# Optimization experiments

Measured on AMD Instinct MI355X. Metric: run time of the kernel, lower is better.

The kernel has to match this reference:

```python
import jax, jax.numpy as jnp
import numpy as np

# ---- module hyperparameters (from init_kwargs) ----
DIM = 16        # Hilbert-space dimension (density matrix is DIM x DIM)
BATCH = 32      # number of initial states evolved in parallel
K_LIND = 4      # number of Lindblad collapse operators
N_TS = 512      # number of Euler integration steps
N_CTRLS = 4     # number of control channels
N_PARAMS = 16   # B-spline control points per channel
DEGREE = 3      # cubic B-splines
T_TOTAL = 1.0
DT = T_TOTAL / N_TS


def _bspline_basis_matrix(t, knots, degree):
    """Cox-de Boor recursion, vectorized over all basis functions.
    t: (n_ts,), knots: (n_knots,). Returns (n_ts, n_knots-1-degree)."""
    k = knots
    # degree-0: indicator of half-open knot spans -> (n_ts, n_knots-1)
    B = ((k[None, :-1] <= t[:, None]) & (t[:, None] < k[None, 1:])).astype(t.dtype)
    for d in range(1, degree + 1):
        left_den = k[d:-1] - k[:-(d + 1)]
        right_den = k[d + 1:] - k[1:-d]
        left = jnp.where(left_den > 0,
                         (t[:, None] - k[None, :-(d + 1)]) / jnp.where(left_den > 0, left_den, 1.0) * B[:, :-1],
                         0.0)
        right = jnp.where(right_den > 0,
                          (k[None, d + 1:] - t[:, None]) / jnp.where(right_den > 0, right_den, 1.0) * B[:, 1:],
                          0.0)
        B = left + right
    return B  # (n_ts, n_knots - 1 - degree) == (n_ts, N_PARAMS)


def setup_inputs() -> dict:
    key = jax.random.key(0)
    ks = jax.random.split(key, 10)
    f32 = jnp.float32
    params = 0.5 * jax.random.normal(ks[0], (N_PARAMS, N_CTRLS), f32)
    H0_re = jax.random.normal(ks[1], (DIM, DIM), f32)
    H0_im = jax.random.normal(ks[2], (DIM, DIM), f32)
    Hc_re = jax.random.normal(ks[3], (N_CTRLS, DIM, DIM), f32)
    Hc_im = jax.random.normal(ks[4], (N_CTRLS, DIM, DIM), f32)
    L_re = 0.3 * jax.random.normal(ks[5], (K_LIND, DIM, DIM), f32)
    L_im = 0.3 * jax.random.normal(ks[6], (K_LIND, DIM, DIM), f32)
    # valid density matrices: rho0 = A A^dag / tr(A A^dag)
    A = (jax.random.normal(ks[7], (BATCH, DIM, DIM), f32)
         + 1j * jax.random.normal(ks[8], (BATCH, DIM, DIM), f32)).astype(jnp.complex64)
    rho0 = jnp.einsum('bij,bkj->bik', A, A.conj())
    tr = jnp.trace(rho0, axis1=-2, axis2=-1).real[:, None, None]
    rho0 = rho0 / tr.astype(jnp.complex64)
    return {
        'params': params,
        'H0_re': H0_re, 'H0_im': H0_im,
        'Hc_re': Hc_re, 'Hc_im': Hc_im,
        'L_re': L_re, 'L_im': L_im,
        'rho0_re': jnp.real(rho0).astype(f32),
        'rho0_im': jnp.imag(rho0).astype(f32),
    }


def reference(params, H0_re, H0_im, Hc_re, Hc_im, L_re, L_im, rho0_re, rho0_im):
    c64 = jnp.complex64
    # Hermitize Hamiltonians
    H0 = (H0_re + 1j * H0_im).astype(c64)
    H0 = 0.5 * (H0 + H0.conj().T)
    Hc = (Hc_re + 1j * Hc_im).astype(c64)
    Hc = 0.5 * (Hc + jnp.conj(jnp.swapaxes(Hc, -1, -2)))
    L = (L_re + 1j * L_im).astype(c64)              # (K, d, d)
    LdL = jnp.einsum('kji,kjl->il', L.conj(), L)    # sum_k L^dag L  (d, d)
    rho0 = (rho0_re + 1j * rho0_im).astype(c64)     # (B, d, d)

    # B-spline control pulses (clamped knot vector, as in evaluate_bspline_batch)
    t = jnp.arange(N_TS, dtype=jnp.float32) * DT
    knots = jnp.concatenate([
        jnp.zeros(DEGREE, jnp.float32),
        jnp.linspace(0.0, T_TOTAL, N_PARAMS - DEGREE + 1).astype(jnp.float32),
        T_TOTAL * jnp.ones(DEGREE, jnp.float32),
    ])
    basis = _bspline_basis_matrix(t, knots, DEGREE)  # (n_ts, n_params)
    u = basis @ params                               # (n_ts, n_ctrls)

    def step(rho, u_t):
        H = H0 + jnp.einsum('c,cij->ij', u_t.astype(c64), Hc)
        jump = jnp.einsum('kij,bjl,kml->bim', L, rho, L.conj())
        drho = (-1j) * (H @ rho - rho @ H) + jump - 0.5 * (LdL @ rho + rho @ LdL)
        rho_new = rho + DT * drho
        pops = jnp.real(jnp.diagonal(rho_new, axis1=-2, axis2=-1)).astype(jnp.float32)
        return rho_new, pops

    _, pops = jax.lax.scan(step, rho0, u)
    return pops  # (n_ts, batch, dim) real populations
```

## Files before the change

### kernel.cpp

```cpp
#include <hip/hip_runtime.h>
#include <hip/hip_bf16.h>

#define DIM    16
#define BATCH  32
#define KL     4
#define NTS    512
#define NC     4
#define NPAR   16
#define DTF    (1.0f/512.0f)
#define BST    40
#define FST    20

using short8  = __attribute__((ext_vector_type(8))) short;
using short4v = __attribute__((ext_vector_type(4))) short;
using f32x4   = __attribute__((ext_vector_type(4))) float;

__device__ __forceinline__ float b2f(__hip_bfloat16 x) { return __bfloat162float(x); }

__device__ __forceinline__ float ldval(const void* p, int idx, bool isf32) {
  return isf32 ? ((const float*)p)[idx]
               : __bfloat162float(((const __hip_bfloat16*)p)[idx]);
}
__device__ __forceinline__ unsigned short f2bf(float x) {
  unsigned u = __float_as_uint(x);
  unsigned r = u + 0x7FFFu + ((u >> 16) & 1u);
  return (unsigned short)(r >> 16);
}
__device__ __forceinline__ float bf2f(unsigned short h) {
  return __uint_as_float(((unsigned)h) << 16);
}
__device__ __forceinline__ void split2(float v, unsigned short& h, unsigned short& l) {
  unsigned u = __float_as_uint(v);
  h = (unsigned short)(u >> 16);
  float r = v - __uint_as_float(u & 0xFFFF0000u);
  l = (unsigned short)(__float_as_uint(r) >> 16);
}
__device__ __forceinline__ short8 ldfrag(const unsigned short* p) {
  return *(const short8*)p;
}
__device__ __forceinline__ short8 negbf8(short8 a) {
  union { short8 s; unsigned u[4]; } v; v.s = a;
  #pragma unroll
  for (int q = 0; q < 4; ++q) v.u[q] ^= 0x80008000u;
  return v.s;
}
__device__ __forceinline__ f32x4 mm3(short8 Ah, short8 Al, short8 Bh, short8 Bl, f32x4 acc) {
  acc = __builtin_amdgcn_mfma_f32_16x16x32_bf16(Ah, Bh, acc, 0, 0, 0);
  acc = __builtin_amdgcn_mfma_f32_16x16x32_bf16(Al, Bh, acc, 0, 0, 0);
  acc = __builtin_amdgcn_mfma_f32_16x16x32_bf16(Ah, Bl, acc, 0, 0, 0);
  return acc;
}
__device__ __forceinline__ void packfrag(const float* v, short8& hi, short8& lo) {
  union { short8 s; unsigned short e[8]; } H, L;
  #pragma unroll
  for (int q = 0; q < 8; ++q) split2(v[q], H.e[q], L.e[q]);
  hi = H.s; lo = L.s;
}

__global__ __launch_bounds__(512, 1)
void lindblad_evolve(const void* __restrict__ g_params,
                     const void* __restrict__ g_H0re, const void* __restrict__ g_H0im,
                     const void* __restrict__ g_Hcre, const void* __restrict__ g_Hcim,
                     const void* __restrict__ g_Lre,  const void* __restrict__ g_Lim,
                     const void* __restrict__ g_r0re, const void* __restrict__ g_r0im,
                     float* __restrict__ g_out)
{
  __shared__ __align__(16) unsigned short sPh[16*BST], sPl[16*BST];
  __shared__ __align__(16) unsigned short sTh[KL][16*BST], sTl[KL][16*BST];
  __shared__ __align__(16) unsigned short sLh[KL][16*BST], sLl[KL][16*BST];
  __shared__ __align__(16) float sMr[16*FST],  sMi[16*FST];
  __shared__ __align__(16) float sMrT[16*FST], sMiT[16*FST];
  __shared__ __align__(16) float sU[NTS][NC];
  __shared__ __align__(16) float sPops[NTS*DIM];
  __shared__ int sFlag;

  const int tid = threadIdx.x;
  const int b   = blockIdx.x;
  const int i   = tid >> 4;
  const int j   = tid & 15;
  const int wv  = tid >> 6;
  const int ln  = tid & 63;
  const int fm  = ln & 15;
  const int fq  = ln >> 4;
  const int row0 = fq * 4;
  const int fOff  = fm*BST + fq*8;
  const int fOffS = fm*BST + ((fq*8 + 16) & 31);

  if (tid == 0) sFlag = 0;
  __syncthreads();
  if (tid < 256) {
    float v = b2f(((const __hip_bfloat16*)g_H0re)[tid]);
    if (!(fabsf(v) <= 1e10f)) atomicOr(&sFlag, 1);
  }
  __syncthreads();
  const bool isf32 = (sFlag != 0);

  {
    float kn[20];
    kn[0] = 0.f; kn[1] = 0.f; kn[2] = 0.f;
    #pragma unroll
    for (int q = 0; q < 14; ++q) kn[3 + q] = (float)q / 13.0f;
    kn[17] = 1.f; kn[18] = 1.f; kn[19] = 1.f;
    const int ts = tid;
    const float t = (float)ts * DTF;
    float B[19];
    #pragma unroll
    for (int q = 0; q < 19; ++q) B[q] = (kn[q] <= t && t < kn[q+1]) ? 1.f : 0.f;
    #pragma unroll
    for (int d = 1; d <= 3; ++d) {
      #pragma unroll
      for (int q = 0; q + d < 19; ++q) {
        float ld = kn[q+d]   - kn[q];
        float rd = kn[q+d+1] - kn[q+1];
        float lv = (ld > 0.f) ? (t - kn[q])     / ld * B[q]   : 0.f;
        float rv = (rd > 0.f) ? (kn[q+d+1] - t) / rd * B[q+1] : 0.f;
        B[q] = lv + rv;
      }
    }
    #pragma unroll
    for (int c = 0; c < NC; ++c) {
      float s = 0.f;
      #pragma unroll
      for (int q = 0; q < NPAR; ++q) s += B[q] * ldval(g_params, q*NC + c, isf32);
      sU[ts][c] = s;
    }
  }

  if (tid < 256) {
    float* scr = sPops;
    const int ij = i*16 + j, ji = j*16 + i;
    float h0r = 0.5f * (ldval(g_H0re, ij, isf32) + ldval(g_H0re, ji, isf32));
    float h0i = 0.5f * (ldval(g_H0im, ij, isf32) - ldval(g_H0im, ji, isf32));
    float ldr = 0.f, ldi = 0.f;
    for (int k = 0; k < KL; ++k) {
      #pragma unroll
      for (int m = 0; m < DIM; ++m) {
        float ar = ldval(g_Lre, k*256 + m*16 + i, isf32), ai = ldval(g_Lim, k*256 + m*16 + i, isf32);
        float br = ldval(g_Lre, k*256 + m*16 + j, isf32), bi = ldval(g_Lim, k*256 + m*16 + j, isf32);
        ldr += ar*br + ai*bi;
        ldi += ar*bi - ai*br;
      }
    }
    scr[0*256 + ij] =  h0i - 0.5f*ldr;
    scr[1*256 + ij] = -h0r - 0.5f*ldi;
    #pragma unroll
    for (int c = 0; c < NC; ++c) {
      float hr = 0.5f * (ldval(g_Hcre, c*256 + ij, isf32) + ldval(g_Hcre, c*256 + ji, isf32));
      float hi = 0.5f * (ldval(g_Hcim, c*256 + ij, isf32) - ldval(g_Hcim, c*256 + ji, isf32));
      scr[(2 + 2*c)*256 + ij] =  hi;
      scr[(3 + 2*c)*256 + ij] = -hr;
    }
    #pragma unroll
    for (int k = 0; k < KL; ++k) {
      float lr = ldval(g_Lre, k*256 + ij, isf32);
      float li = ldval(g_Lim, k*256 + ij, isf32);
      unsigned short h;
      h = f2bf(lr); sLh[k][i*BST + j]      = h; sLl[k][i*BST + j]      = f2bf(lr - bf2f(h));
      h = f2bf(li); sLh[k][i*BST + 16 + j] = h; sLl[k][i*BST + 16 + j] = f2bf(li - bf2f(h));
    }
    float r0 = ldval(g_r0re, b*256 + ij, isf32);
    float m0 = ldval(g_r0im, b*256 + ij, isf32);
    unsigned short h, l;
    split2(r0, h, l); sPh[j*BST + i]      = h; sPl[j*BST + i]      = l;
    split2(m0, h, l); sPh[j*BST + 16 + i] = h; sPl[j*BST + 16 + i] = l;
  }

  __syncthreads();

  short8 Ah, Al;
  short8 JBh[KL], JBl[KL];
  float  G0v[8], Gcv[NC][8];
  float  rm[4] = {0.f,0.f,0.f,0.f};

  if (wv < 2) {
    const int comp = (fq < 2) ? 0 : 1;
    const int base = (fq & 1) * 8;
    const float* scr = sPops;
    {
      const float* s0 = &scr[comp*256 + fm*16 + base];
      f32x4 va = *(const f32x4*)s0, vb = *(const f32x4*)(s0 + 4);
      G0v[0]=va[0]; G0v[1]=va[1]; G0v[2]=va[2]; G0v[3]=va[3];
      G0v[4]=vb[0]; G0v[5]=vb[1]; G0v[6]=vb[2]; G0v[7]=vb[3];
    }
    #pragma unroll
    for (int c = 0; c < NC; ++c) {
      const float* s0 = &scr[(2 + 2*c + comp)*256 + fm*16 + base];
      f32x4 va = *(const f32x4*)s0, vb = *(const f32x4*)(s0 + 4);
      Gcv[c][0]=va[0]; Gcv[c][1]=va[1]; Gcv[c][2]=va[2]; Gcv[c][3]=va[3];
      Gcv[c][4]=vb[0]; Gcv[c][5]=vb[1]; Gcv[c][6]=vb[2]; Gcv[c][7]=vb[3];
    }
    f32x4 uv = *(const f32x4*)&sU[0][0];
    float gv[8];
    #pragma unroll
    for (int q = 0; q < 8; ++q)
      gv[q] = G0v[q] + uv[0]*Gcv[0][q] + uv[1]*Gcv[1][q] + uv[2]*Gcv[2][q] + uv[3]*Gcv[3][q];
    packfrag(gv, Ah, Al);
  } else if (wv < 6) {
    const int k = wv - 2;
    Ah = ldfrag(&sLh[k][fOff]);
    Al = ldfrag(&sLl[k][fOff]);
  } else if (wv == 6) {
    #pragma unroll
    for (int k = 0; k < KL; ++k) { JBh[k] = ldfrag(&sLh[k][fOff]); JBl[k] = ldfrag(&sLl[k][fOff]); }
    #pragma unroll
    for (int q = 0; q < 4; ++q) rm[q] = ldval(g_r0re, b*256 + (row0+q)*16 + fm, isf32);
  } else {
    #pragma unroll
    for (int k = 0; k < KL; ++k) {
      short8 h = ldfrag(&sLh[k][fOffS]);
      short8 l = ldfrag(&sLl[k][fOffS]);
      if (fq < 2) { h = negbf8(h); l = negbf8(l); }
      JBh[k] = h; JBl[k] = l;
    }
    #pragma unroll
    for (int q = 0; q < 4; ++q) rm[q] = ldval(g_r0im, b*256 + (row0+q)*16 + fm, isf32);
  }

  #pragma unroll 1
  for (int t = 0; t < NTS; ++t) {
    __syncthreads();

    if (wv < 2) {
      short8 Bh, Bl;
      if (wv == 0) {
        Bh = ldfrag(&sPh[fOff]);  Bl = ldfrag(&sPl[fOff]);
        if (fq >= 2) { Bh = negbf8(Bh); Bl = negbf8(Bl); }
      } else {
        Bh = ldfrag(&sPh[fOffS]); Bl = ldfrag(&sPl[fOffS]);
      }
      f32x4 a = {0.f,0.f,0.f,0.f};
      a = mm3(Ah, Al, Bh, Bl, a);
      float* Mn = (wv == 0) ? sMr  : sMi;
      float* Mt = (wv == 0) ? sMrT : sMiT;
      #pragma unroll
      for (int r = 0; r < 4; ++r) Mn[(row0 + r)*FST + fm] = a[r];
      *(f32x4*)&Mt[fm*FST + row0] = a;
      const int tn = (t + 1 < NTS) ? (t + 1) : t;
      f32x4 uv = *(const f32x4*)&sU[tn][0];
      float gv[8];
      #pragma unroll
      for (int q = 0; q < 8; ++q)
        gv[q] = G0v[q] + uv[0]*Gcv[0][q] + uv[1]*Gcv[1][q] + uv[2]*Gcv[2][q] + uv[3]*Gcv[3][q];
      packfrag(gv, Ah, Al);
    } else if (wv < 6) {
      const int k = wv - 2;
      short8 Brh = ldfrag(&sPh[fOff]),  Brl = ldfrag(&sPl[fOff]);
      if (fq >= 2) { Brh = negbf8(Brh); Brl = negbf8(Brl); }
      short8 Bih = ldfrag(&sPh[fOffS]), Bil = ldfrag(&sPl[fOffS]);
      f32x4 ar = {0.f,0.f,0.f,0.f}, ai = {0.f,0.f,0.f,0.f};
      ar = mm3(Ah, Al, Brh, Brl, ar);
      ai = mm3(Ah, Al, Bih, Bil, ai);
      #pragma unroll
      for (int r = 0; r < 4; ++r) {
        unsigned short h, l;
        split2(ar[r], h, l);
        sTh[k][(row0 + r)*BST + fm]      = h;
        sTl[k][(row0 + r)*BST + fm]      = l;
        split2(ai[r], h, l);
        sTh[k][(row0 + r)*BST + 16 + fm] = h;
        sTl[k][(row0 + r)*BST + 16 + fm] = l;
      }
    }

    __syncthreads();

    if (wv >= 6) {
      f32x4 a0 = {0.f,0.f,0.f,0.f}, a1 = {0.f,0.f,0.f,0.f},
            a2 = {0.f,0.f,0.f,0.f}, a3 = {0.f,0.f,0.f,0.f};
      a0 = mm3(ldfrag(&sTh[0][fOff]), ldfrag(&sTl[0][fOff]), JBh[0], JBl[0], a0);
      a1 = mm3(ldfrag(&sTh[1][fOff]), ldfrag(&sTl[1][fOff]), JBh[1], JBl[1], a1);
      a2 = mm3(ldfrag(&sTh[2][fOff]), ldfrag(&sTl[2][fOff]), JBh[2], JBl[2], a2);
      a3 = mm3(ldfrag(&sTh[3][fOff]), ldfrag(&sTl[3][fOff]), JBh[3], JBl[3], a3);
      const float* Mt = (wv == 6) ? sMrT : sMiT;
      const float* Mn = (wv == 6) ? sMr  : sMi;
      f32x4 d1 = *(const f32x4*)&Mt[fm*FST + row0];
      f32x4 d2 = *(const f32x4*)&Mn[fm*FST + row0];
      union { short4v s; unsigned short e[4]; } HH, LL;
      if (wv == 6) {
        #pragma unroll
        for (int q = 0; q < 4; ++q) {
          rm[q] += DTF * (d1[q] + d2[q] + ((a0[q] + a1[q]) + (a2[q] + a3[q])));
          split2(rm[q], HH.e[q], LL.e[q]);
        }
        *(short4v*)&sPh[fm*BST + row0] = HH.s;
        *(short4v*)&sPl[fm*BST + row0] = LL.s;
        if ((unsigned)(fm - row0) < 4u) sPops[t*DIM + fm] = rm[fm - row0];
      } else {
        #pragma unroll
        for (int q = 0; q < 4; ++q) {
          rm[q] += DTF * (d1[q] - d2[q] + ((a0[q] + a1[q]) + (a2[q] + a3[q])));
          split2(rm[q], HH.e[q], LL.e[q]);
        }
        *(short4v*)&sPh[fm*BST + 16 + row0] = HH.s;
        *(short4v*)&sPl[fm*BST + 16 + row0] = LL.s;
      }
    }
  }

  __syncthreads();
  #pragma unroll
  for (int s = 0; s < NTS*DIM/512; ++s) {
    int idx = s*512 + tid;
    g_out[(idx >> 4)*(BATCH*DIM) + b*DIM + (idx & 15)] = sPops[idx];
  }
}

extern "C" void kernel_launch(void* const* d_in, const int* in_sizes, int n_in,
                              void* d_out, int out_size, void* d_ws, size_t ws_size,
                              hipStream_t stream) {
  (void)out_size; (void)d_ws; (void)ws_size;
  const void *P, *H0r, *H0i, *Hcr, *Hci, *Lr, *Li, *R0r, *R0i;
  int idx64 = -1;
  for (int q = 0; q < n_in; ++q) if (in_sizes[q] == 64) idx64 = q;
  if (idx64 == 6) {
    H0i = d_in[0]; H0r = d_in[1];
    Hci = d_in[2]; Hcr = d_in[3];
    Li  = d_in[4]; Lr  = d_in[5];
    P   = d_in[6];
    R0i = d_in[7]; R0r = d_in[8];
  } else {
    P   = d_in[0];
    H0r = d_in[1]; H0i = d_in[2];
    Hcr = d_in[3]; Hci = d_in[4];
    Lr  = d_in[5]; Li  = d_in[6];
    R0r = d_in[7]; R0i = d_in[8];
  }
  lindblad_evolve<<<dim3(BATCH), dim3(512), 0, stream>>>(
      P, H0r, H0i, Hcr, Hci, Lr, Li, R0r, R0i, (float*)d_out);
}
```

Before: 422.1 us.

## Fold final update into Hamiltonian waves and rebalance jump products across waves

After: 441.1 us. 1.04x slower.

```diff
diff --git a/kernel.cpp b/kernel.cpp
--- a/kernel.cpp
+++ b/kernel.cpp
@@ -10,6 +10,7 @@
 #define DTF    (1.0f/512.0f)
 #define BST    40
 #define FST    20
+#define TST    36
 
 using short8  = __attribute__((ext_vector_type(8))) short;
 using short4v = __attribute__((ext_vector_type(4))) short;
@@ -35,6 +36,11 @@
   float r = v - __uint_as_float(u & 0xFFFF0000u);
   l = (unsigned short)(__float_as_uint(r) >> 16);
 }
+__device__ __forceinline__ unsigned splitpack(float v) {
+  unsigned short h, l;
+  split2(v, h, l);
+  return (unsigned)h | ((unsigned)l << 16);
+}
 __device__ __forceinline__ short8 ldfrag(const unsigned short* p) {
   return *(const short8*)p;
 }
@@ -54,6 +60,20 @@
   union { short8 s; unsigned short e[8]; } H, L;
   #pragma unroll
   for (int q = 0; q < 8; ++q) split2(v[q], H.e[q], L.e[q]);
+  hi = H.s; lo = L.s;
+}
+__device__ __forceinline__ void ldfrag_paired(const unsigned* p, short8& hi, short8& lo) {
+  uint4 wa = *(const uint4*)p;
+  uint4 wb = *(const uint4*)(p + 4);
+  union { short8 s; unsigned u[4]; } H, L;
+  H.u[0] = __builtin_amdgcn_perm(wa.y, wa.x, 0x05040100u);
+  H.u[1] = __builtin_amdgcn_perm(wa.w, wa.z, 0x05040100u);
+  H.u[2] = __builtin_amdgcn_perm(wb.y, wb.x, 0x05040100u);
+  H.u[3] = __builtin_amdgcn_perm(wb.w, wb.z, 0x05040100u);
+  L.u[0] = __builtin_amdgcn_perm(wa.y, wa.x, 0x07060302u);
+  L.u[1] = __builtin_amdgcn_perm(wa.w, wa.z, 0x07060302u);
+  L.u[2] = __builtin_amdgcn_perm(wb.y, wb.x, 0x07060302u);
+  L.u[3] = __builtin_amdgcn_perm(wb.w, wb.z, 0x07060302u);
   hi = H.s; lo = L.s;
 }
 
@@ -66,10 +86,9 @@
                      float* __restrict__ g_out)
 {
   __shared__ __align__(16) unsigned short sPh[16*BST], sPl[16*BST];
-  __shared__ __align__(16) unsigned short sTh[KL][16*BST], sTl[KL][16*BST];
+  __shared__ __align__(16) unsigned sTp[KL][16*TST];
   __shared__ __align__(16) unsigned short sLh[KL][16*BST], sLl[KL][16*BST];
-  __shared__ __align__(16) float sMr[16*FST],  sMi[16*FST];
-  __shared__ __align__(16) float sMrT[16*FST], sMiT[16*FST];
+  __shared__ __align__(16) float sMr[16*FST], sMi[16*FST];
   __shared__ __align__(16) float sU[NTS][NC];
   __shared__ __align__(16) float sPops[NTS*DIM];
   __shared__ int sFlag;
@@ -101,8 +120,7 @@
     #pragma unroll
     for (int q = 0; q < 14; ++q) kn[3 + q] = (float)q / 13.0f;
     kn[17] = 1.f; kn[18] = 1.f; kn[19] = 1.f;
-    const int ts = tid;
-    const float t = (float)ts * DTF;
+    const float t = (float)tid * DTF;
     float B[19];
     #pragma unroll
     for (int q = 0; q < 19; ++q) B[q] = (kn[q] <= t && t < kn[q+1]) ? 1.f : 0.f;
@@ -122,7 +140,7 @@
       float s = 0.f;
       #pragma unroll
       for (int q = 0; q < NPAR; ++q) s += B[q] * ldval(g_params, q*NC + c, isf32);
-      sU[ts][c] = s;
+      sU[tid][c] = s;
     }
   }
 
@@ -179,15 +197,15 @@
     {
       const float* s0 = &scr[comp*256 + fm*16 + base];
       f32x4 va = *(const f32x4*)s0, vb = *(const f32x4*)(s0 + 4);
-      G0v[0]=va[0]; G0v[1]=va[1]; G0v[2]=va[2]; G0v[3]=va[3];
-      G0v[4]=vb[0]; G0v[5]=vb[1]; G0v[6]=vb[2]; G0v[7]=vb[3];
+      #pragma unroll
+      for (int q = 0; q < 4; ++q) { G0v[q] = va[q]; G0v[4+q] = vb[q]; }
     }
     #pragma unroll
     for (int c = 0; c < NC; ++c) {
       const float* s0 = &scr[(2 + 2*c + comp)*256 + fm*16 + base];
       f32x4 va = *(const f32x4*)s0, vb = *(const f32x4*)(s0 + 4);
-      Gcv[c][0]=va[0]; Gcv[c][1]=va[1]; Gcv[c][2]=va[2]; Gcv[c][3]=va[3];
-      Gcv[c][4]=vb[0]; Gcv[c][5]=vb[1]; Gcv[c][6]=vb[2]; Gcv[c][7]=vb[3];
+      #pragma unroll
+      for (int q = 0; q < 4; ++q) { Gcv[c][q] = va[q]; Gcv[c][4+q] = vb[q]; }
     }
     f32x4 uv = *(const f32x4*)&sU[0][0];
     float gv[8];
@@ -195,31 +213,33 @@
     for (int q = 0; q < 8; ++q)
       gv[q] = G0v[q] + uv[0]*Gcv[0][q] + uv[1]*Gcv[1][q] + uv[2]*Gcv[2][q] + uv[3]*Gcv[3][q];
     packfrag(gv, Ah, Al);
-  } else if (wv < 6) {
-    const int k = wv - 2;
+    if (wv == 0) {
+      #pragma unroll
+      for (int k = 0; k < KL; ++k) { JBh[k] = ldfrag(&sLh[k][fOff]); JBl[k] = ldfrag(&sLl[k][fOff]); }
+      #pragma unroll
+      for (int q = 0; q < 4; ++q) rm[q] = ldval(g_r0re, b*256 + (row0+q)*16 + fm, isf32);
+    } else {
+      #pragma unroll
+      for (int k = 0; k < KL; ++k) {
+        short8 h = ldfrag(&sLh[k][fOffS]);
+        short8 l = ldfrag(&sLl[k][fOffS]);
+        if (fq < 2) { h = negbf8(h); l = negbf8(l); }
+        JBh[k] = h; JBl[k] = l;
+      }
+      #pragma unroll
+      for (int q = 0; q < 4; ++q) rm[q] = ldval(g_r0im, b*256 + (row0+q)*16 + fm, isf32);
+    }
+  } else {
+    const int k = (wv < 6) ? (wv - 2) : (wv - 4);
     Ah = ldfrag(&sLh[k][fOff]);
     Al = ldfrag(&sLl[k][fOff]);
-  } else if (wv == 6) {
-    #pragma unroll
-    for (int k = 0; k < KL; ++k) { JBh[k] = ldfrag(&sLh[k][fOff]); JBl[k] = ldfrag(&sLl[k][fOff]); }
-    #pragma unroll
-    for (int q = 0; q < 4; ++q) rm[q] = ldval(g_r0re, b*256 + (row0+q)*16 + fm, isf32);
-  } else {
-    #pragma unroll
-    for (int k = 0; k < KL; ++k) {
-      short8 h = ldfrag(&sLh[k][fOffS]);
-      short8 l = ldfrag(&sLl[k][fOffS]);
-      if (fq < 2) { h = negbf8(h); l = negbf8(l); }
-      JBh[k] = h; JBl[k] = l;
-    }
-    #pragma unroll
-    for (int q = 0; q < 4; ++q) rm[q] = ldval(g_r0im, b*256 + (row0+q)*16 + fm, isf32);
   }
 
   #pragma unroll 1
   for (int t = 0; t < NTS; ++t) {
     __syncthreads();
 
+    f32x4 d1 = {0.f,0.f,0.f,0.f};
     if (wv < 2) {
       short8 Bh, Bl;
       if (wv == 0) {
@@ -228,13 +248,10 @@
       } else {
         Bh = ldfrag(&sPh[fOffS]); Bl = ldfrag(&sPl[fOffS]);
       }
-      f32x4 a = {0.f,0.f,0.f,0.f};
-      a = mm3(Ah, Al, Bh, Bl, a);
-      float* Mn = (wv == 0) ? sMr  : sMi;
-      float* Mt = (wv == 0) ? sMrT : sMiT;
-      #pragma unroll
-      for (int r = 0; r < 4; ++r) Mn[(row0 + r)*FST + fm] = a[r];
-      *(f32x4*)&Mt[fm*FST + row0] = a;
+      d1 = mm3(Ah, Al, Bh, Bl, d1);
+      float* Mn = (wv == 0) ? sMr : sMi;
+      #pragma unroll
+      for (int r = 0; r < 4; ++r) Mn[(row0 + r)*FST + fm] = d1[r];
       const int tn = (t + 1 < NTS) ? (t + 1) : t;
       f32x4 uv = *(const f32x4*)&sU[tn][0];
       float gv[8];
@@ -242,41 +259,54 @@
       for (int q = 0; q < 8; ++q)
         gv[q] = G0v[q] + uv[0]*Gcv[0][q] + uv[1]*Gcv[1][q] + uv[2]*Gcv[2][q] + uv[3]*Gcv[3][q];
       packfrag(gv, Ah, Al);
-    } else if (wv < 6) {
-      const int k = wv - 2;
-      short8 Brh = ldfrag(&sPh[fOff]),  Brl = ldfrag(&sPl[fOff]);
-      if (fq >= 2) { Brh = negbf8(Brh); Brl = negbf8(Brl); }
-      short8 Bih = ldfrag(&sPh[fOffS]), Bil = ldfrag(&sPl[fOffS]);
-      f32x4 ar = {0.f,0.f,0.f,0.f}, ai = {0.f,0.f,0.f,0.f};
-      ar = mm3(Ah, Al, Brh, Brl, ar);
-      ai = mm3(Ah, Al, Bih, Bil, ai);
-      #pragma unroll
-      for (int r = 0; r < 4; ++r) {
-        unsigned short h, l;
-        split2(ar[r], h, l);
-        sTh[k][(row0 + r)*BST + fm]      = h;
-        sTl[k][(row0 + r)*BST + fm]      = l;
-        split2(ai[r], h, l);
-        sTh[k][(row0 + r)*BST + 16 + fm] = h;
-        sTl[k][(row0 + r)*BST + 16 + fm] = l;
+    } else {
+      const int k = (wv < 6) ? (wv - 2) : (wv - 4);
+      if (wv < 4) {
+        short8 Brh = ldfrag(&sPh[fOff]),  Brl = ldfrag(&sPl[fOff]);
+        if (fq >= 2) { Brh = negbf8(Brh); Brl = negbf8(Brl); }
+        short8 Bih = ldfrag(&sPh[fOffS]), Bil = ldfrag(&sPl[fOffS]);
+        f32x4 ar = {0.f,0.f,0.f,0.f}, ai = {0.f,0.f,0.f,0.f};
+        ar = mm3(Ah, Al, Brh, Brl, ar);
+        ai = mm3(Ah, Al, Bih, Bil, ai);
+        #pragma unroll
+        for (int r = 0; r < 4; ++r) {
+          sTp[k][(row0 + r)*TST + fm]      = splitpack(ar[r]);
+          sTp[k][(row0 + r)*TST + 16 + fm] = splitpack(ai[r]);
+        }
+      } else if (wv < 6) {
+        short8 Bh = ldfrag(&sPh[fOff]), Bl = ldfrag(&sPl[fOff]);
+        if (fq >= 2) { Bh = negbf8(Bh); Bl = negbf8(Bl); }
+        f32x4 a = {0.f,0.f,0.f,0.f};
+        a = mm3(Ah, Al, Bh, Bl, a);
+        #pragma unroll
+        for (int r = 0; r < 4; ++r) sTp[k][(row0 + r)*TST + fm] = splitpack(a[r]);
+      } else {
+        short8 Bh = ldfrag(&sPh[fOffS]), Bl = ldfrag(&sPl[fOffS]);
+        f32x4 a = {0.f,0.f,0.f,0.f};
+        a = mm3(Ah, Al, Bh, Bl, a);
+        #pragma unroll
+        for (int r = 0; r < 4; ++r) sTp[k][(row0 + r)*TST + 16 + fm] = splitpack(a[r]);
       }
     }
 
     __syncthreads();
 
-    if (wv >= 6) {
+    if (wv < 2) {
+      short8 T0h, T0l, T1h, T1l, T2h, T2l, T3h, T3l;
+      ldfrag_paired(&sTp[0][fm*TST + fq*8], T0h, T0l);
+      ldfrag_paired(&sTp[1][fm*TST + fq*8], T1h, T1l);
+      ldfrag_paired(&sTp[2][fm*TST + fq*8], T2h, T2l);
+      ldfrag_paired(&sTp[3][fm*TST + fq*8], T3h, T3l);
       f32x4 a0 = {0.f,0.f,0.f,0.f}, a1 = {0.f,0.f,0.f,0.f},
             a2 = {0.f,0.f,0.f,0.f}, a3 = {0.f,0.f,0.f,0.f};
-      a0 = mm3(ldfrag(&sTh[0][fOff]), ldfrag(&sTl[0][fOff]), JBh[0], JBl[0], a0);
-      a1 = mm3(ldfrag(&sTh[1][fOff]), ldfrag(&sTl[1][fOff]), JBh[1], JBl[1], a1);
-      a2 = mm3(ldfrag(&sTh[2][fOff]), ldfrag(&sTl[2][fOff]), JBh[2], JBl[2], a2);
-      a3 = mm3(ldfrag(&sTh[3][fOff]), ldfrag(&sTl[3][fOff]), JBh[3], JBl[3], a3);
-      const float* Mt = (wv == 6) ? sMrT : sMiT;
-      const float* Mn = (wv == 6) ? sMr  : sMi;
-      f32x4 d1 = *(const f32x4*)&Mt[fm*FST + row0];
+      a0 = mm3(T0h, T0l, JBh[0], JBl[0], a0);
+      a1 = mm3(T1h, T1l, JBh[1], JBl[1], a1);
+      a2 = mm3(T2h, T2l, JBh[2], JBl[2], a2);
+      a3 = mm3(T3h, T3l, JBh[3], JBl[3], a3);
+      const float* Mn = (wv == 0) ? sMr : sMi;
       f32x4 d2 = *(const f32x4*)&Mn[fm*FST + row0];
       union { short4v s; unsigned short e[4]; } HH, LL;
-      if (wv == 6) {
+      if (wv == 0) {
         #pragma unroll
         for (int q = 0; q < 4; ++q) {
           rm[q] += DTF * (d1[q] + d2[q] + ((a0[q] + a1[q]) + (a2[q] + a3[q])));
```

## Rebalance per-step MFMA work across all eight waves with an extra stage

Applied to the files above, without the earlier changes.

Measured after the change: 477.0 us. 1.13x slower.

```diff
diff --git a/kernel.cpp b/kernel.cpp
--- a/kernel.cpp
+++ b/kernel.cpp
@@ -70,14 +70,13 @@
   __shared__ __align__(16) unsigned short sLh[KL][16*BST], sLl[KL][16*BST];
   __shared__ __align__(16) float sMr[16*FST],  sMi[16*FST];
   __shared__ __align__(16) float sMrT[16*FST], sMiT[16*FST];
+  __shared__ __align__(16) float sJT[4][16*FST];
   __shared__ __align__(16) float sU[NTS][NC];
   __shared__ __align__(16) float sPops[NTS*DIM];
   __shared__ int sFlag;
 
   const int tid = threadIdx.x;
   const int b   = blockIdx.x;
-  const int i   = tid >> 4;
-  const int j   = tid & 15;
   const int wv  = tid >> 6;
   const int ln  = tid & 63;
   const int fm  = ln & 15;
@@ -101,8 +100,7 @@
     #pragma unroll
     for (int q = 0; q < 14; ++q) kn[3 + q] = (float)q / 13.0f;
     kn[17] = 1.f; kn[18] = 1.f; kn[19] = 1.f;
-    const int ts = tid;
-    const float t = (float)ts * DTF;
+    const float t = (float)tid * DTF;
     float B[19];
     #pragma unroll
     for (int q = 0; q < 19; ++q) B[q] = (kn[q] <= t && t < kn[q+1]) ? 1.f : 0.f;
@@ -122,12 +120,13 @@
       float s = 0.f;
       #pragma unroll
       for (int q = 0; q < NPAR; ++q) s += B[q] * ldval(g_params, q*NC + c, isf32);
-      sU[ts][c] = s;
+      sU[tid][c] = s;
     }
   }
 
   if (tid < 256) {
     float* scr = sPops;
+    const int i = tid >> 4, j = tid & 15;
     const int ij = i*16 + j, ji = j*16 + i;
     float h0r = 0.5f * (ldval(g_H0re, ij, isf32) + ldval(g_H0re, ji, isf32));
     float h0i = 0.5f * (ldval(g_H0im, ij, isf32) - ldval(g_H0im, ji, isf32));
@@ -168,7 +167,8 @@
   __syncthreads();
 
   short8 Ah, Al;
-  short8 JBh[KL], JBl[KL];
+  short8 A2h, A2l;
+  short8 JBh[2], JBl[2];
   float  G0v[8], Gcv[NC][8];
   float  rm[4] = {0.f,0.f,0.f,0.f};
 
@@ -179,15 +179,15 @@
     {
       const float* s0 = &scr[comp*256 + fm*16 + base];
       f32x4 va = *(const f32x4*)s0, vb = *(const f32x4*)(s0 + 4);
-      G0v[0]=va[0]; G0v[1]=va[1]; G0v[2]=va[2]; G0v[3]=va[3];
-      G0v[4]=vb[0]; G0v[5]=vb[1]; G0v[6]=vb[2]; G0v[7]=vb[3];
+      #pragma unroll
+      for (int q = 0; q < 4; ++q) { G0v[q] = va[q]; G0v[4+q] = vb[q]; }
     }
     #pragma unroll
     for (int c = 0; c < NC; ++c) {
       const float* s0 = &scr[(2 + 2*c + comp)*256 + fm*16 + base];
       f32x4 va = *(const f32x4*)s0, vb = *(const f32x4*)(s0 + 4);
-      Gcv[c][0]=va[0]; Gcv[c][1]=va[1]; Gcv[c][2]=va[2]; Gcv[c][3]=va[3];
-      Gcv[c][4]=vb[0]; Gcv[c][5]=vb[1]; Gcv[c][6]=vb[2]; Gcv[c][7]=vb[3];
+      #pragma unroll
+      for (int q = 0; q < 4; ++q) { Gcv[c][q] = va[q]; Gcv[c][4+q] = vb[q]; }
     }
     f32x4 uv = *(const f32x4*)&sU[0][0];
     float gv[8];
@@ -195,46 +195,126 @@
     for (int q = 0; q < 8; ++q)
       gv[q] = G0v[q] + uv[0]*Gcv[0][q] + uv[1]*Gcv[1][q] + uv[2]*Gcv[2][q] + uv[3]*Gcv[3][q];
     packfrag(gv, Ah, Al);
-  } else if (wv < 6) {
-    const int k = wv - 2;
-    Ah = ldfrag(&sLh[k][fOff]);
-    Al = ldfrag(&sLl[k][fOff]);
-  } else if (wv == 6) {
-    #pragma unroll
-    for (int k = 0; k < KL; ++k) { JBh[k] = ldfrag(&sLh[k][fOff]); JBl[k] = ldfrag(&sLl[k][fOff]); }
-    #pragma unroll
-    for (int q = 0; q < 4; ++q) rm[q] = ldval(g_r0re, b*256 + (row0+q)*16 + fm, isf32);
+    A2h = ldfrag(&sLh[3][fOff]);
+    A2l = ldfrag(&sLl[3][fOff]);
   } else {
-    #pragma unroll
-    for (int k = 0; k < KL; ++k) {
-      short8 h = ldfrag(&sLh[k][fOffS]);
-      short8 l = ldfrag(&sLl[k][fOffS]);
-      if (fq < 2) { h = negbf8(h); l = negbf8(l); }
-      JBh[k] = h; JBl[k] = l;
-    }
-    #pragma unroll
-    for (int q = 0; q < 4; ++q) rm[q] = ldval(g_r0im, b*256 + (row0+q)*16 + fm, isf32);
+    const int kA = (wv >> 1) - 1;
+    Ah = ldfrag(&sLh[kA][fOff]);
+    Al = ldfrag(&sLl[kA][fOff]);
+    if (wv < 6) {
+      const int k0 = (wv < 4) ? 0 : 2;
+      if ((wv & 1) == 0) {
+        JBh[0] = ldfrag(&sLh[k0][fOff]);   JBl[0] = ldfrag(&sLl[k0][fOff]);
+        JBh[1] = ldfrag(&sLh[k0+1][fOff]); JBl[1] = ldfrag(&sLl[k0+1][fOff]);
+      } else {
+        #pragma unroll
+        for (int kk = 0; kk < 2; ++kk) {
+          short8 h = ldfrag(&sLh[k0+kk][fOffS]);
+          short8 l = ldfrag(&sLl[k0+kk][fOffS]);
+          if (fq < 2) { h = negbf8(h); l = negbf8(l); }
+          JBh[kk] = h; JBl[kk] = l;
+        }
+      }
+    }
+    if (wv == 6) {
+      #pragma unroll
+      for (int q = 0; q < 4; ++q) rm[q] = ldval(g_r0re, b*256 + (row0+q)*16 + fm, isf32);
+    } else if (wv == 7) {
+      #pragma unroll
+      for (int q = 0; q < 4; ++q) rm[q] = ldval(g_r0im, b*256 + (row0+q)*16 + fm, isf32);
+    }
   }
 
   #pragma unroll 1
   for (int t = 0; t < NTS; ++t) {
     __syncthreads();
 
-    if (wv < 2) {
+    {
       short8 Bh, Bl;
-      if (wv == 0) {
+      if ((wv & 1) == 0) {
         Bh = ldfrag(&sPh[fOff]);  Bl = ldfrag(&sPl[fOff]);
         if (fq >= 2) { Bh = negbf8(Bh); Bl = negbf8(Bl); }
       } else {
         Bh = ldfrag(&sPh[fOffS]); Bl = ldfrag(&sPl[fOffS]);
       }
-      f32x4 a = {0.f,0.f,0.f,0.f};
-      a = mm3(Ah, Al, Bh, Bl, a);
-      float* Mn = (wv == 0) ? sMr  : sMi;
-      float* Mt = (wv == 0) ? sMrT : sMiT;
-      #pragma unroll
-      for (int r = 0; r < 4; ++r) Mn[(row0 + r)*FST + fm] = a[r];
-      *(f32x4*)&Mt[fm*FST + row0] = a;
+      if (wv < 2) {
+        f32x4 aM = {0.f,0.f,0.f,0.f}, aT = {0.f,0.f,0.f,0.f};
+        aM = mm3(Ah, Al, Bh, Bl, aM);
+        aT = mm3(A2h, A2l, Bh, Bl, aT);
+        float* Mn = (wv == 0) ? sMr  : sMi;
+        float* Mt = (wv == 0) ? sMrT : sMiT;
+        #pragma unroll
+        for (int r = 0; r < 4; ++r) Mn[(row0 + r)*FST + fm] = aM[r];
+        *(f32x4*)&Mt[fm*FST + row0] = aM;
+        const int co = (wv == 0) ? 0 : 16;
+        #pragma unroll
+        for (int r = 0; r < 4; ++r) {
+          unsigned short h, l;
+          split2(aT[r], h, l);
+          sTh[3][(row0 + r)*BST + co + fm] = h;
+          sTl[3][(row0 + r)*BST + co + fm] = l;
+        }
+      } else {
+        const int kT = (wv >> 1) - 1;
+        const int co = (wv & 1) ? 16 : 0;
+        f32x4 aT = {0.f,0.f,0.f,0.f};
+        aT = mm3(Ah, Al, Bh, Bl, aT);
+        #pragma unroll
+        for (int r = 0; r < 4; ++r) {
+          unsigned short h, l;
+          split2(aT[r], h, l);
+          sTh[kT][(row0 + r)*BST + co + fm] = h;
+          sTl[kT][(row0 + r)*BST + co + fm] = l;
+        }
+      }
+    }
+
+    __syncthreads();
+
+    if (wv >= 2 && wv < 6) {
+      const int k0 = (wv < 4) ? 0 : 2;
+      short8 TaH = ldfrag(&sTh[k0][fOff]),   TaL = ldfrag(&sTl[k0][fOff]);
+      short8 TbH = ldfrag(&sTh[k0+1][fOff]), TbL = ldfrag(&sTl[k0+1][fOff]);
+      f32x4 pa = {0.f,0.f,0.f,0.f}, pb = {0.f,0.f,0.f,0.f};
+      pa = mm3(TaH, TaL, JBh[0], JBl[0], pa);
+      pb = mm3(TbH, TbL, JBh[1], JBl[1], pb);
+      f32x4 p;
+      #pragma unroll
+      for (int q = 0; q < 4; ++q) p[q] = pa[q] + pb[q];
+      const int pd = ((wv & 1) << 1) | ((wv >> 2) & 1);
+      *(f32x4*)&sJT[pd][fm*FST + row0] = p;
+    }
+
+    __syncthreads();
+
+    if (wv == 6) {
+      f32x4 d1  = *(const f32x4*)&sMrT[fm*FST + row0];
+      f32x4 d2  = *(const f32x4*)&sMr [fm*FST + row0];
+      f32x4 p01 = *(const f32x4*)&sJT[0][fm*FST + row0];
+      f32x4 p23 = *(const f32x4*)&sJT[1][fm*FST + row0];
+      union { short4v s; unsigned short e[4]; } HH, LL;
+      #pragma unroll
+      for (int q = 0; q < 4; ++q) {
+        rm[q] += DTF * (d1[q] + d2[q] + (p01[q] + p23[q]));
+        split2(rm[q], HH.e[q], LL.e[q]);
+      }
+      *(short4v*)&sPh[fm*BST + row0] = HH.s;
+      *(short4v*)&sPl[fm*BST + row0] = LL.s;
+      if ((unsigned)(fm - row0) < 4u) sPops[t*DIM + fm] = rm[fm - row0];
+    } else if (wv == 7) {
+      f32x4 d1  = *(const f32x4*)&sMiT[fm*FST + row0];
+      f32x4 d2  = *(const f32x4*)&sMi [fm*FST + row0];
+      f32x4 p01 = *(const f32x4*)&sJT[2][fm*FST + row0];
+      f32x4 p23 = *(const f32x4*)&sJT[3][fm*FST + row0];
+      union { short4v s; unsigned short e[4]; } HH, LL;
+      #pragma unroll
+      for (int q = 0; q < 4; ++q) {
+        rm[q] += DTF * (d1[q] - d2[q] + (p01[q] + p23[q]));
+        split2(rm[q], HH.e[q], LL.e[q]);
+      }
+      *(short4v*)&sPh[fm*BST + 16 + row0] = HH.s;
+      *(short4v*)&sPl[fm*BST + 16 + row0] = LL.s;
+    } else if (wv < 2) {
       const int tn = (t + 1 < NTS) ? (t + 1) : t;
       f32x4 uv = *(const f32x4*)&sU[tn][0];
       float gv[8];
@@ -242,66 +322,15 @@
       for (int q = 0; q < 8; ++q)
         gv[q] = G0v[q] + uv[0]*Gcv[0][q] + uv[1]*Gcv[1][q] + uv[2]*Gcv[2][q] + uv[3]*Gcv[3][q];
       packfrag(gv, Ah, Al);
-    } else if (wv < 6) {
-      const int k = wv - 2;
-      short8 Brh = ldfrag(&sPh[fOff]),  Brl = ldfrag(&sPl[fOff]);
-      if (fq >= 2) { Brh = negbf8(Brh); Brl = negbf8(Brl); }
-      short8 Bih = ldfrag(&sPh[fOffS]), Bil = ldfrag(&sPl[fOffS]);
-      f32x4 ar = {0.f,0.f,0.f,0.f}, ai = {0.f,0.f,0.f,0.f};
-      ar = mm3(Ah, Al, Brh, Brl, ar);
-      ai = mm3(Ah, Al, Bih, Bil, ai);
-      #pragma unroll
-      for (int r = 0; r < 4; ++r) {
-        unsigned short h, l;
-        split2(ar[r], h, l);
-        sTh[k][(row0 + r)*BST + fm]      = h;
-        sTl[k][(row0 + r)*BST + fm]      = l;
-        split2(ai[r], h, l);
-        sTh[k][(row0 + r)*BST + 16 + fm] = h;
-        sTl[k][(row0 + r)*BST + 16 + fm] = l;
-      }
-    }
-
-    __syncthreads();
-
-    if (wv >= 6) {
-      f32x4 a0 = {0.f,0.f,0.f,0.f}, a1 = {0.f,0.f,0.f,0.f},
-            a2 = {0.f,0.f,0.f,0.f}, a3 = {0.f,0.f,0.f,0.f};
-      a0 = mm3(ldfrag(&sTh[0][fOff]), ldfrag(&sTl[0][fOff]), JBh[0], JBl[0], a0);
-      a1 = mm3(ldfrag(&sTh[1][fOff]), ldfrag(&sTl[1][fOff]), JBh[1], JBl[1], a1);
-      a2 = mm3(ldfrag(&sTh[2][fOff]), ldfrag(&sTl[2][fOff]), JBh[2], JBl[2], a2);
-      a3 = mm3(ldfrag(&sTh[3][fOff]), ldfrag(&sTl[3][fOff]), JBh[3], JBl[3], a3);
-      const float* Mt = (wv == 6) ? sMrT : sMiT;
-      const float* Mn = (wv == 6) ? sMr  : sMi;
-      f32x4 d1 = *(const f32x4*)&Mt[fm*FST + row0];
-      f32x4 d2 = *(const f32x4*)&Mn[fm*FST + row0];
-      union { short4v s; unsigned short e[4]; } HH, LL;
-      if (wv == 6) {
-        #pragma unroll
-        for (int q = 0; q < 4; ++q) {
-          rm[q] += DTF * (d1[q] + d2[q] + ((a0[q] + a1[q]) + (a2[q] + a3[q])));
-          split2(rm[q], HH.e[q], LL.e[q]);
-        }
-        *(short4v*)&sPh[fm*BST + row0] = HH.s;
-        *(short4v*)&sPl[fm*BST + row0] = LL.s;
-        if ((unsigned)(fm - row0) < 4u) sPops[t*DIM + fm] = rm[fm - row0];
-      } else {
-        #pragma unroll
-        for (int q = 0; q < 4; ++q) {
-          rm[q] += DTF * (d1[q] - d2[q] + ((a0[q] + a1[q]) + (a2[q] + a3[q])));
-          split2(rm[q], HH.e[q], LL.e[q]);
-        }
-        *(short4v*)&sPh[fm*BST + 16 + row0] = HH.s;
-        *(short4v*)&sPl[fm*BST + 16 + row0] = LL.s;
-      }
     }
   }
 
   __syncthreads();
   #pragma unroll
-  for (int s = 0; s < NTS*DIM/512; ++s) {
-    int idx = s*512 + tid;
-    g_out[(idx >> 4)*(BATCH*DIM) + b*DIM + (idx & 15)] = sPops[idx];
+  for (int s = 0; s < NTS*DIM/(512*4); ++s) {
+    int idx = (s*512 + tid) * 4;
+    int tt = idx >> 4, dd = idx & 15;
+    *(float4*)&g_out[tt*(BATCH*DIM) + b*DIM + dd] = *(const float4*)&sPops[idx];
   }
 }
 
```

## Restructure jump-term matmul operand roles, overlap H update, vectorize output stores

Applied to the files above, without the earlier changes.

New measurement: 416.9 us. About the same (-1.2%).

```diff
diff --git a/kernel.cpp b/kernel.cpp
--- a/kernel.cpp
+++ b/kernel.cpp
@@ -76,8 +76,6 @@
 
   const int tid = threadIdx.x;
   const int b   = blockIdx.x;
-  const int i   = tid >> 4;
-  const int j   = tid & 15;
   const int wv  = tid >> 6;
   const int ln  = tid & 63;
   const int fm  = ln & 15;
@@ -101,8 +99,7 @@
     #pragma unroll
     for (int q = 0; q < 14; ++q) kn[3 + q] = (float)q / 13.0f;
     kn[17] = 1.f; kn[18] = 1.f; kn[19] = 1.f;
-    const int ts = tid;
-    const float t = (float)ts * DTF;
+    const float t = (float)tid * DTF;
     float B[19];
     #pragma unroll
     for (int q = 0; q < 19; ++q) B[q] = (kn[q] <= t && t < kn[q+1]) ? 1.f : 0.f;
@@ -122,12 +119,13 @@
       float s = 0.f;
       #pragma unroll
       for (int q = 0; q < NPAR; ++q) s += B[q] * ldval(g_params, q*NC + c, isf32);
-      sU[ts][c] = s;
+      sU[tid][c] = s;
     }
   }
 
   if (tid < 256) {
     float* scr = sPops;
+    const int i = tid >> 4, j = tid & 15;
     const int ij = i*16 + j, ji = j*16 + i;
     float h0r = 0.5f * (ldval(g_H0re, ij, isf32) + ldval(g_H0re, ji, isf32));
     float h0i = 0.5f * (ldval(g_H0im, ij, isf32) - ldval(g_H0im, ji, isf32));
@@ -168,6 +166,7 @@
   __syncthreads();
 
   short8 Ah, Al;
+  short8 TrBh, TrBl, TiBh, TiBl;
   short8 JBh[KL], JBl[KL];
   float  G0v[8], Gcv[NC][8];
   float  rm[4] = {0.f,0.f,0.f,0.f};
@@ -179,15 +178,15 @@
     {
       const float* s0 = &scr[comp*256 + fm*16 + base];
       f32x4 va = *(const f32x4*)s0, vb = *(const f32x4*)(s0 + 4);
-      G0v[0]=va[0]; G0v[1]=va[1]; G0v[2]=va[2]; G0v[3]=va[3];
-      G0v[4]=vb[0]; G0v[5]=vb[1]; G0v[6]=vb[2]; G0v[7]=vb[3];
+      #pragma unroll
+      for (int q = 0; q < 4; ++q) { G0v[q] = va[q]; G0v[4+q] = vb[q]; }
     }
     #pragma unroll
     for (int c = 0; c < NC; ++c) {
       const float* s0 = &scr[(2 + 2*c + comp)*256 + fm*16 + base];
       f32x4 va = *(const f32x4*)s0, vb = *(const f32x4*)(s0 + 4);
-      Gcv[c][0]=va[0]; Gcv[c][1]=va[1]; Gcv[c][2]=va[2]; Gcv[c][3]=va[3];
-      Gcv[c][4]=vb[0]; Gcv[c][5]=vb[1]; Gcv[c][6]=vb[2]; Gcv[c][7]=vb[3];
+      #pragma unroll
+      for (int q = 0; q < 4; ++q) { Gcv[c][q] = va[q]; Gcv[c][4+q] = vb[q]; }
     }
     f32x4 uv = *(const f32x4*)&sU[0][0];
     float gv[8];
@@ -197,8 +196,10 @@
     packfrag(gv, Ah, Al);
   } else if (wv < 6) {
     const int k = wv - 2;
-    Ah = ldfrag(&sLh[k][fOff]);
-    Al = ldfrag(&sLl[k][fOff]);
+    TiBh = ldfrag(&sLh[k][fOff]);
+    TiBl = ldfrag(&sLl[k][fOff]);
+    TrBh = (fq >= 2) ? negbf8(TiBh) : TiBh;
+    TrBl = (fq >= 2) ? negbf8(TiBl) : TiBl;
   } else if (wv == 6) {
     #pragma unroll
     for (int k = 0; k < KL; ++k) { JBh[k] = ldfrag(&sLh[k][fOff]); JBl[k] = ldfrag(&sLl[k][fOff]); }
@@ -235,42 +236,38 @@
       #pragma unroll
       for (int r = 0; r < 4; ++r) Mn[(row0 + r)*FST + fm] = a[r];
       *(f32x4*)&Mt[fm*FST + row0] = a;
-      const int tn = (t + 1 < NTS) ? (t + 1) : t;
-      f32x4 uv = *(const f32x4*)&sU[tn][0];
-      float gv[8];
-      #pragma unroll
-      for (int q = 0; q < 8; ++q)
-        gv[q] = G0v[q] + uv[0]*Gcv[0][q] + uv[1]*Gcv[1][q] + uv[2]*Gcv[2][q] + uv[3]*Gcv[3][q];
-      packfrag(gv, Ah, Al);
     } else if (wv < 6) {
       const int k = wv - 2;
-      short8 Brh = ldfrag(&sPh[fOff]),  Brl = ldfrag(&sPl[fOff]);
-      if (fq >= 2) { Brh = negbf8(Brh); Brl = negbf8(Brl); }
-      short8 Bih = ldfrag(&sPh[fOffS]), Bil = ldfrag(&sPl[fOffS]);
-      f32x4 ar = {0.f,0.f,0.f,0.f}, ai = {0.f,0.f,0.f,0.f};
-      ar = mm3(Ah, Al, Brh, Brl, ar);
-      ai = mm3(Ah, Al, Bih, Bil, ai);
+      short8 Arh = ldfrag(&sPh[fOff]),  Arl = ldfrag(&sPl[fOff]);
+      short8 Aih = ldfrag(&sPh[fOffS]), Ail = ldfrag(&sPl[fOffS]);
+      f32x4 tr = {0.f,0.f,0.f,0.f}, ti = {0.f,0.f,0.f,0.f};
+      tr = mm3(Arh, Arl, TrBh, TrBl, tr);
+      ti = mm3(Aih, Ail, TiBh, TiBl, ti);
+      union { short4v s; unsigned short e[4]; } HR, LR, HI, LI;
       #pragma unroll
       for (int r = 0; r < 4; ++r) {
-        unsigned short h, l;
-        split2(ar[r], h, l);
-        sTh[k][(row0 + r)*BST + fm]      = h;
-        sTl[k][(row0 + r)*BST + fm]      = l;
-        split2(ai[r], h, l);
-        sTh[k][(row0 + r)*BST + 16 + fm] = h;
-        sTl[k][(row0 + r)*BST + 16 + fm] = l;
-      }
+        split2(tr[r], HR.e[r], LR.e[r]);
+        split2(ti[r], HI.e[r], LI.e[r]);
+      }
+      *(short4v*)&sTh[k][fm*BST + row0]      = HR.s;
+      *(short4v*)&sTl[k][fm*BST + row0]      = LR.s;
+      *(short4v*)&sTh[k][fm*BST + 16 + row0] = HI.s;
+      *(short4v*)&sTl[k][fm*BST + 16 + row0] = LI.s;
     }
 
     __syncthreads();
 
     if (wv >= 6) {
+      short8 T0h = ldfrag(&sTh[0][fOff]), T0l = ldfrag(&sTl[0][fOff]);
+      short8 T1h = ldfrag(&sTh[1][fOff]), T1l = ldfrag(&sTl[1][fOff]);
+      short8 T2h = ldfrag(&sTh[2][fOff]), T2l = ldfrag(&sTl[2][fOff]);
+      short8 T3h = ldfrag(&sTh[3][fOff]), T3l = ldfrag(&sTl[3][fOff]);
       f32x4 a0 = {0.f,0.f,0.f,0.f}, a1 = {0.f,0.f,0.f,0.f},
             a2 = {0.f,0.f,0.f,0.f}, a3 = {0.f,0.f,0.f,0.f};
-      a0 = mm3(ldfrag(&sTh[0][fOff]), ldfrag(&sTl[0][fOff]), JBh[0], JBl[0], a0);
-      a1 = mm3(ldfrag(&sTh[1][fOff]), ldfrag(&sTl[1][fOff]), JBh[1], JBl[1], a1);
-      a2 = mm3(ldfrag(&sTh[2][fOff]), ldfrag(&sTl[2][fOff]), JBh[2], JBl[2], a2);
-      a3 = mm3(ldfrag(&sTh[3][fOff]), ldfrag(&sTl[3][fOff]), JBh[3], JBl[3], a3);
+      a0 = mm3(JBh[0], JBl[0], T0h, T0l, a0);
+      a1 = mm3(JBh[1], JBl[1], T1h, T1l, a1);
+      a2 = mm3(JBh[2], JBl[2], T2h, T2l, a2);
+      a3 = mm3(JBh[3], JBl[3], T3h, T3l, a3);
       const float* Mt = (wv == 6) ? sMrT : sMiT;
       const float* Mn = (wv == 6) ? sMr  : sMi;
       f32x4 d1 = *(const f32x4*)&Mt[fm*FST + row0];
@@ -288,20 +285,29 @@
       } else {
         #pragma unroll
         for (int q = 0; q < 4; ++q) {
-          rm[q] += DTF * (d1[q] - d2[q] + ((a0[q] + a1[q]) + (a2[q] + a3[q])));
+          rm[q] += DTF * (d1[q] - d2[q] - ((a0[q] + a1[q]) + (a2[q] + a3[q])));
           split2(rm[q], HH.e[q], LL.e[q]);
         }
         *(short4v*)&sPh[fm*BST + 16 + row0] = HH.s;
         *(short4v*)&sPl[fm*BST + 16 + row0] = LL.s;
       }
+    } else if (wv < 2) {
+      const int tn = (t + 1 < NTS) ? (t + 1) : t;
+      f32x4 uv = *(const f32x4*)&sU[tn][0];
+      float gv[8];
+      #pragma unroll
+      for (int q = 0; q < 8; ++q)
+        gv[q] = G0v[q] + uv[0]*Gcv[0][q] + uv[1]*Gcv[1][q] + uv[2]*Gcv[2][q] + uv[3]*Gcv[3][q];
+      packfrag(gv, Ah, Al);
     }
   }
 
   __syncthreads();
   #pragma unroll
-  for (int s = 0; s < NTS*DIM/512; ++s) {
-    int idx = s*512 + tid;
-    g_out[(idx >> 4)*(BATCH*DIM) + b*DIM + (idx & 15)] = sPops[idx];
+  for (int s = 0; s < NTS*DIM/(512*4); ++s) {
+    int idx = (s*512 + tid) * 4;
+    int tt = idx >> 4, dd = idx & 15;
+    *(float4*)&g_out[tt*(BATCH*DIM) + b*DIM + dd] = *(const float4*)&sPops[idx];
   }
 }
 
```
